# Kernel tuning notes

Hardware: AMD Instinct MI355X
Metric: run time of the kernel (lower is better)

## Reference

```python
import jax, jax.numpy as jnp
import numpy as np

N_NODES = 100000
N_EDGES = 1600000
D_FEAT = 128
N_CLASS = 40
K_HOPS = 2  # nlayers


def setup_inputs() -> dict:
    key = jax.random.key(0)
    k1, k2, k3, k4, k5 = jax.random.split(key, 5)
    src = jax.random.randint(k1, (N_EDGES,), 0, N_NODES)
    dst = jax.random.randint(k2, (N_EDGES,), 0, N_NODES)
    features = jax.random.normal(k3, (N_NODES, D_FEAT), dtype=jnp.float32)
    # positive edge weights (EdgeWeightNorm requires nonnegative)
    edge_weight = jax.random.uniform(k4, (N_EDGES,), dtype=jnp.float32, minval=0.1, maxval=1.0)
    W = jax.random.normal(k5, (D_FEAT, N_CLASS), dtype=jnp.float32) / np.float32(np.sqrt(D_FEAT))
    b = jnp.zeros((N_CLASS,), dtype=jnp.float32)
    return {"features": features, "src": src, "dst": dst,
            "edge_weight": edge_weight, "W": W, "b": b}


def reference(features, src, dst, edge_weight, W, b):
    """SGConv (DGL) with edge_weight: EdgeWeightNorm('both') then k SpMM hops, then fc."""
    n = features.shape[0]
    # EdgeWeightNorm('both'): w_ij / sqrt(out_deg_w(src_i) * in_deg_w(dst_j))
    out_deg = jax.ops.segment_sum(edge_weight, src, num_segments=n)  # weighted out-degree
    in_deg = jax.ops.segment_sum(edge_weight, dst, num_segments=n)   # weighted in-degree
    w = edge_weight * jax.lax.rsqrt(out_deg[src]) * jax.lax.rsqrt(in_deg[dst])  # [E]
    h = features
    for _ in range(K_HOPS):
        # message = h[src] * w ; aggregate = scatter-sum over dst
        h = jax.ops.segment_sum(h[src] * w[:, None], dst, num_segments=n)  # [N, D]
    return h @ W + b  # fc projection [N, C]
```

## Files before the change

### kernel.cpp

```cpp
#include <hip/hip_runtime.h>

#define N_NODES 100000
#define N_EDGES 1600000
#define D_FEAT  128
#define N_CLASS 40
#define ELL_CAP 48

#define QS  10239.6875f
#define DQ  9.765923e-5f
#define FSC  2048.0f
#define FINV (1.0f/2048.0f)
#define CNT_SHIFT 20
#define W_MASK ((1u << CNT_SHIFT) - 1u)

#define RSZ 20000
#define NR 5
#define SLICES 32
#define EPS (N_EDGES/SLICES)
#define HB (NR*SLICES)

#define GEMM2_T ((N_NODES/2)*(N_CLASS/4))
#define GEMM2_B ((GEMM2_T + 1023)/1024)

#define NCH 5

__device__ __forceinline__ float bf_lo(unsigned int u) { return __uint_as_float(u << 16); }
__device__ __forceinline__ float bf_hi(unsigned int u) { return __uint_as_float(u & 0xFFFF0000u); }
__device__ __forceinline__ unsigned int bf_pack2(float a, float b) {
    unsigned int ua = __float_as_uint(a), ub = __float_as_uint(b);
    ua = (ua + 0x7FFFu + ((ua >> 16) & 1u)) >> 16;
    ub = (ub + 0x7FFFu + ((ub >> 16) & 1u)) & 0xFFFF0000u;
    return ua | ub;
}

__global__ __launch_bounds__(1024) void mega1_kernel(
    const int* __restrict__ src, const int* __restrict__ dst, const float* __restrict__ ew,
    const float* __restrict__ f, const float* __restrict__ W,
    unsigned int* __restrict__ dhist, unsigned int* __restrict__ shist,
    unsigned int* __restrict__ g0)
{
    __shared__ unsigned int smem[RSZ];
    const int b = blockIdx.x;
    const int tid = threadIdx.x;

    if (b < 2 * HB) {
        const bool isDst = (b < HB);
        const int b2 = isDst ? b : b - HB;
        const int* idxarr = isDst ? dst : src;
        unsigned int* outh = isDst ? dhist : shist;
        int r = b2 / SLICES, s = b2 - r * SLICES;
        int nb = r * RSZ;
        for (int i = tid; i < RSZ; i += 1024) smem[i] = 0u;
        __syncthreads();
        int e0 = s * EPS;
        const int4*   idx4 = (const int4*)(idxarr + e0);
        const float4* ew4  = (const float4*)(ew + e0);
        const unsigned int cbit = isDst ? (1u << CNT_SHIFT) : 0u;
        for (int i = tid; i < EPS / 8; i += 1024) {
            int4   ia = idx4[2 * i],     ib = idx4[2 * i + 1];
            float4 wa = ew4[2 * i],      wb = ew4[2 * i + 1];
            unsigned int r0 = (unsigned int)(ia.x - nb);
            unsigned int r1 = (unsigned int)(ia.y - nb);
            unsigned int r2 = (unsigned int)(ia.z - nb);
            unsigned int r3 = (unsigned int)(ia.w - nb);
            unsigned int r4 = (unsigned int)(ib.x - nb);
            unsigned int r5 = (unsigned int)(ib.y - nb);
            unsigned int r6 = (unsigned int)(ib.z - nb);
            unsigned int r7 = (unsigned int)(ib.w - nb);
            if (r0 < RSZ) atomicAdd(&smem[r0], cbit | (unsigned int)(wa.x * FSC + 0.5f));
            if (r1 < RSZ) atomicAdd(&smem[r1], cbit | (unsigned int)(wa.y * FSC + 0.5f));
            if (r2 < RSZ) atomicAdd(&smem[r2], cbit | (unsigned int)(wa.z * FSC + 0.5f));
            if (r3 < RSZ) atomicAdd(&smem[r3], cbit | (unsigned int)(wa.w * FSC + 0.5f));
            if (r4 < RSZ) atomicAdd(&smem[r4], cbit | (unsigned int)(wb.x * FSC + 0.5f));
            if (r5 < RSZ) atomicAdd(&smem[r5], cbit | (unsigned int)(wb.y * FSC + 0.5f));
            if (r6 < RSZ) atomicAdd(&smem[r6], cbit | (unsigned int)(wb.z * FSC + 0.5f));
            if (r7 < RSZ) atomicAdd(&smem[r7], cbit | (unsigned int)(wb.w * FSC + 0.5f));
        }
        __syncthreads();
        unsigned int* o = outh + (size_t)b2 * RSZ;
        for (int i = tid; i < RSZ; i += 1024) o[i] = smem[i];
    } else {
        float* Ws = (float*)smem;
        for (int i = tid; i < D_FEAT * N_CLASS; i += 1024) Ws[i] = W[i];
        __syncthreads();
        int idx = (b - 2 * HB) * 1024 + tid;
        if (idx >= GEMM2_T) return;
        int n2 = idx / (N_CLASS / 4);
        int c4i = idx - n2 * (N_CLASS / 4);
        int c4 = c4i * 4;
        int n0 = n2 * 2;
        const float* fr0 = f + (size_t)n0 * D_FEAT;
        const float* fr1 = fr0 + D_FEAT;
        float4 acc0 = {0.f, 0.f, 0.f, 0.f};
        float4 acc1 = {0.f, 0.f, 0.f, 0.f};
#pragma unroll 1
        for (int kq = 0; kq < D_FEAT; kq += 4) {
            float4 fv0 = *(const float4*)(fr0 + kq);
            float4 fv1 = *(const float4*)(fr1 + kq);
#pragma unroll
            for (int j = 0; j < 4; ++j) {
                float fa = (j == 0) ? fv0.x : (j == 1) ? fv0.y : (j == 2) ? fv0.z : fv0.w;
                float fb = (j == 0) ? fv1.x : (j == 1) ? fv1.y : (j == 2) ? fv1.z : fv1.w;
                const float4 wv = *(const float4*)&Ws[(kq + j) * N_CLASS + c4];
                acc0.x = fmaf(fa, wv.x, acc0.x); acc0.y = fmaf(fa, wv.y, acc0.y);
                acc0.z = fmaf(fa, wv.z, acc0.z); acc0.w = fmaf(fa, wv.w, acc0.w);
                acc1.x = fmaf(fb, wv.x, acc1.x); acc1.y = fmaf(fb, wv.y, acc1.y);
                acc1.z = fmaf(fb, wv.z, acc1.z); acc1.w = fmaf(fb, wv.w, acc1.w);
            }
        }
        uint2 p0, p1;
        p0.x = bf_pack2(acc0.x, acc0.y); p0.y = bf_pack2(acc0.z, acc0.w);
        p1.x = bf_pack2(acc1.x, acc1.y); p1.y = bf_pack2(acc1.z, acc1.w);
        *(uint2*)&g0[(size_t)n0 * (N_CLASS / 2) + c4i * 2] = p0;
        *(uint2*)&g0[(size_t)(n0 + 1) * (N_CLASS / 2) + c4i * 2] = p1;
    }
}

__global__ void scan_kernel(const unsigned int* __restrict__ dhist,
                            const unsigned int* __restrict__ shist,
                            unsigned char* __restrict__ base8, int* __restrict__ cnt,
                            float* __restrict__ rs_out, float* __restrict__ rs_in,
                            unsigned int* __restrict__ ell)
{
    int n = blockIdx.x * 256 + threadIdx.x;
    if (n >= N_NODES) return;
    int r = n / RSZ, off = n - r * RSZ;
    const unsigned int* dp = dhist + (size_t)r * SLICES * RSZ + off;
    const unsigned int* sp = shist + (size_t)r * SLICES * RSZ + off;
    unsigned char* b8 = base8 + (size_t)r * SLICES * RSZ + off;
    unsigned int ow = 0, iw = 0, run = 0;
#pragma unroll
    for (int s = 0; s < SLICES; ++s) {
        unsigned int dv = dp[(size_t)s * RSZ];
        ow += sp[(size_t)s * RSZ];
        b8[(size_t)s * RSZ] = (unsigned char)run;
        run += dv >> CNT_SHIFT;
        iw += dv & W_MASK;
    }
    rs_out[n] = ow ? rsqrtf((float)ow * FINV) : 0.f;
    rs_in[n]  = iw ? rsqrtf((float)iw * FINV) : 0.f;
    cnt[n] = (int)run;
    int k  = min((int)run, ELL_CAP);
    int k8 = min((k + 7) & ~7, ELL_CAP);
    unsigned int* row = ell + (size_t)n * ELL_CAP;
    for (int i = k; i < k8; ++i) row[i] = 0u;
}

__global__ __launch_bounds__(1024) void fill_kernel(
    const int* __restrict__ src, const int* __restrict__ dst, const float* __restrict__ ew,
    const unsigned char* __restrict__ base8, const float* __restrict__ rs_out,
    unsigned int* __restrict__ ell)
{
    __shared__ unsigned int lds[RSZ];
    const int r = blockIdx.x & 7;
    const int s = blockIdx.x >> 3;
    if (r >= NR) return;
    const int tid = threadIdx.x;
    const int b2 = r * SLICES + s;
    int nb = r * RSZ;
    const unsigned int* bp = (const unsigned int*)(base8 + (size_t)b2 * RSZ);
    for (int i = tid; i < RSZ / 4; i += 1024) {
        unsigned int v = bp[i];
        lds[4 * i]     = v & 255u;
        lds[4 * i + 1] = (v >> 8) & 255u;
        lds[4 * i + 2] = (v >> 16) & 255u;
        lds[4 * i + 3] = v >> 24;
    }
    __syncthreads();
    int e0 = s * EPS;
    const int4*   d4 = (const int4*)(dst + e0);
    const int4*   s4 = (const int4*)(src + e0);
    const float4* w4 = (const float4*)(ew + e0);
    for (int i = tid; i < EPS / 8; i += 1024) {
        int4   da = d4[2 * i], db = d4[2 * i + 1];
        int4   sa = s4[2 * i], sb = s4[2 * i + 1];
        float4 wa = w4[2 * i], wb = w4[2 * i + 1];
#pragma unroll
        for (int j = 0; j < 8; ++j) {
            int d, sn; float w;
            switch (j) {
                case 0: d = da.x; sn = sa.x; w = wa.x; break;
                case 1: d = da.y; sn = sa.y; w = wa.y; break;
                case 2: d = da.z; sn = sa.z; w = wa.z; break;
                case 3: d = da.w; sn = sa.w; w = wa.w; break;
                case 4: d = db.x; sn = sb.x; w = wb.x; break;
                case 5: d = db.y; sn = sb.y; w = wb.y; break;
                case 6: d = db.z; sn = sb.z; w = wb.z; break;
                default: d = db.w; sn = sb.w; w = wb.w; break;
            }
            unsigned int rr = (unsigned int)(d - nb);
            if (rr < RSZ) {
                unsigned int slot = atomicAdd(&lds[rr], 1u);
                if (slot < ELL_CAP) {
                    int q = (int)(w * rs_out[sn] * QS + 0.5f);
                    q = q > 32767 ? 32767 : q;
                    ell[(size_t)d * ELL_CAP + slot] = ((unsigned int)sn << 15) | (unsigned int)q;
                }
            }
        }
    }
}

__global__ void hop_kernel(const unsigned int* __restrict__ ell, const int* __restrict__ cnt,
                           const float* __restrict__ rs_in, const unsigned int* __restrict__ gin,
                           void* __restrict__ gout, const float* __restrict__ bias)
{
    int t = blockIdx.x * 256 + threadIdx.x;
    if (t >= N_NODES * NCH) return;
    int n = t / NCH;
    int c8 = t - n * NCH;
    int k = min(cnt[n], ELL_CAP);
    k = (k + 7) & ~7;
    const uint4* row4 = (const uint4*)(ell + (size_t)n * ELL_CAP);
    const uint4* gin4 = (const uint4*)gin;
    float a0 = 0.f, a1 = 0.f, a2 = 0.f, a3 = 0.f, a4 = 0.f, a5 = 0.f, a6 = 0.f, a7 = 0.f;
    for (int i = 0; i < k; i += 8) {
        uint4 v0 = row4[i >> 2];
        uint4 v1 = row4[(i >> 2) + 1];
        unsigned int e0 = v0.x, e1 = v0.y, e2 = v0.z, e3 = v0.w;
        unsigned int e4 = v1.x, e5 = v1.y, e6 = v1.z, e7 = v1.w;
        uint4 g0v = gin4[(size_t)(e0 >> 15) * NCH + c8];
        uint4 g1v = gin4[(size_t)(e1 >> 15) * NCH + c8];
        uint4 g2v = gin4[(size_t)(e2 >> 15) * NCH + c8];
        uint4 g3v = gin4[(size_t)(e3 >> 15) * NCH + c8];
        uint4 g4v = gin4[(size_t)(e4 >> 15) * NCH + c8];
        uint4 g5v = gin4[(size_t)(e5 >> 15) * NCH + c8];
        uint4 g6v = gin4[(size_t)(e6 >> 15) * NCH + c8];
        uint4 g7v = gin4[(size_t)(e7 >> 15) * NCH + c8];
        float w0 = (float)(e0 & 32767u) * DQ;
        float w1 = (float)(e1 & 32767u) * DQ;
        float w2 = (float)(e2 & 32767u) * DQ;
        float w3 = (float)(e3 & 32767u) * DQ;
        float w4 = (float)(e4 & 32767u) * DQ;
        float w5 = (float)(e5 & 32767u) * DQ;
        float w6 = (float)(e6 & 32767u) * DQ;
        float w7 = (float)(e7 & 32767u) * DQ;
        a0 = fmaf(w0, bf_lo(g0v.x), a0); a1 = fmaf(w0, bf_hi(g0v.x), a1);
        a2 = fmaf(w0, bf_lo(g0v.y), a2); a3 = fmaf(w0, bf_hi(g0v.y), a3);
        a4 = fmaf(w0, bf_lo(g0v.z), a4); a5 = fmaf(w0, bf_hi(g0v.z), a5);
        a6 = fmaf(w0, bf_lo(g0v.w), a6); a7 = fmaf(w0, bf_hi(g0v.w), a7);
        a0 = fmaf(w1, bf_lo(g1v.x), a0); a1 = fmaf(w1, bf_hi(g1v.x), a1);
        a2 = fmaf(w1, bf_lo(g1v.y), a2); a3 = fmaf(w1, bf_hi(g1v.y), a3);
        a4 = fmaf(w1, bf_lo(g1v.z), a4); a5 = fmaf(w1, bf_hi(g1v.z), a5);
        a6 = fmaf(w1, bf_lo(g1v.w), a6); a7 = fmaf(w1, bf_hi(g1v.w), a7);
        a0 = fmaf(w2, bf_lo(g2v.x), a0); a1 = fmaf(w2, bf_hi(g2v.x), a1);
        a2 = fmaf(w2, bf_lo(g2v.y), a2); a3 = fmaf(w2, bf_hi(g2v.y), a3);
        a4 = fmaf(w2, bf_lo(g2v.z), a4); a5 = fmaf(w2, bf_hi(g2v.z), a5);
        a6 = fmaf(w2, bf_lo(g2v.w), a6); a7 = fmaf(w2, bf_hi(g2v.w), a7);
        a0 = fmaf(w3, bf_lo(g3v.x), a0); a1 = fmaf(w3, bf_hi(g3v.x), a1);
        a2 = fmaf(w3, bf_lo(g3v.y), a2); a3 = fmaf(w3, bf_hi(g3v.y), a3);
        a4 = fmaf(w3, bf_lo(g3v.z), a4); a5 = fmaf(w3, bf_hi(g3v.z), a5);
        a6 = fmaf(w3, bf_lo(g3v.w), a6); a7 = fmaf(w3, bf_hi(g3v.w), a7);
        a0 = fmaf(w4, bf_lo(g4v.x), a0); a1 = fmaf(w4, bf_hi(g4v.x), a1);
        a2 = fmaf(w4, bf_lo(g4v.y), a2); a3 = fmaf(w4, bf_hi(g4v.y), a3);
        a4 = fmaf(w4, bf_lo(g4v.z), a4); a5 = fmaf(w4, bf_hi(g4v.z), a5);
        a6 = fmaf(w4, bf_lo(g4v.w), a6); a7 = fmaf(w4, bf_hi(g4v.w), a7);
        a0 = fmaf(w5, bf_lo(g5v.x), a0); a1 = fmaf(w5, bf_hi(g5v.x), a1);
        a2 = fmaf(w5, bf_lo(g5v.y), a2); a3 = fmaf(w5, bf_hi(g5v.y), a3);
        a4 = fmaf(w5, bf_lo(g5v.z), a4); a5 = fmaf(w5, bf_hi(g5v.z), a5);
        a6 = fmaf(w5, bf_lo(g5v.w), a6); a7 = fmaf(w5, bf_hi(g5v.w), a7);
        a0 = fmaf(w6, bf_lo(g6v.x), a0); a1 = fmaf(w6, bf_hi(g6v.x), a1);
        a2 = fmaf(w6, bf_lo(g6v.y), a2); a3 = fmaf(w6, bf_hi(g6v.y), a3);
        a4 = fmaf(w6, bf_lo(g6v.z), a4); a5 = fmaf(w6, bf_hi(g6v.z), a5);
        a6 = fmaf(w6, bf_lo(g6v.w), a6); a7 = fmaf(w6, bf_hi(g6v.w), a7);
        a0 = fmaf(w7, bf_lo(g7v.x), a0); a1 = fmaf(w7, bf_hi(g7v.x), a1);
        a2 = fmaf(w7, bf_lo(g7v.y), a2); a3 = fmaf(w7, bf_hi(g7v.y), a3);
        a4 = fmaf(w7, bf_lo(g7v.z), a4); a5 = fmaf(w7, bf_hi(g7v.z), a5);
        a6 = fmaf(w7, bf_lo(g7v.w), a6); a7 = fmaf(w7, bf_hi(g7v.w), a7);
    }
    float sc = rs_in[n];
    a0 *= sc; a1 *= sc; a2 *= sc; a3 *= sc; a4 *= sc; a5 *= sc; a6 *= sc; a7 *= sc;
    if (bias) {
        const float4 b0 = *(const float4*)&bias[c8 * 8];
        const float4 b1 = *(const float4*)&bias[c8 * 8 + 4];
        float4 o0 = {a0 + b0.x, a1 + b0.y, a2 + b0.z, a3 + b0.w};
        float4 o1 = {a4 + b1.x, a5 + b1.y, a6 + b1.z, a7 + b1.w};
        float* op = (float*)gout + (size_t)n * N_CLASS + c8 * 8;
        *(float4*)op = o0;
        *(float4*)(op + 4) = o1;
    } else {
        uint4 p;
        p.x = bf_pack2(a0, a1);
        p.y = bf_pack2(a2, a3);
        p.z = bf_pack2(a4, a5);
        p.w = bf_pack2(a6, a7);
        ((uint4*)gout)[(size_t)n * NCH + c8] = p;
    }
}

extern "C" void kernel_launch(void* const* d_in, const int* in_sizes, int n_in,
                              void* d_out, int out_size, void* d_ws, size_t ws_size,
                              hipStream_t stream) {
    const float* features = (const float*)d_in[0];
    const int*   src      = (const int*)d_in[1];
    const int*   dst      = (const int*)d_in[2];
    const float* ew       = (const float*)d_in[3];
    const float* W        = (const float*)d_in[4];
    const float* b        = (const float*)d_in[5];
    float*       out      = (float*)d_out;

    char* ws = (char*)d_ws;
    unsigned int* dhist = (unsigned int*)ws;  ws += (size_t)HB * RSZ * 4;
    unsigned int* shist = (unsigned int*)ws;  ws += (size_t)HB * RSZ * 4;
    unsigned char* base8 = (unsigned char*)ws; ws += (size_t)HB * RSZ;
    int*   cnt    = (int*)ws;    ws += (size_t)N_NODES * 4;
    float* rs_out = (float*)ws;  ws += (size_t)N_NODES * 4;
    float* rs_in  = (float*)ws;  ws += (size_t)N_NODES * 4;
    unsigned int* ell = (unsigned int*)ws; ws += (size_t)N_NODES * ELL_CAP * 4;
    unsigned int* g0  = (unsigned int*)ws;
    unsigned int* g1  = dhist;

    const int B = 256;

    mega1_kernel<<<2 * HB + GEMM2_B, 1024, 0, stream>>>(
        src, dst, ew, features, W, dhist, shist, g0);
    scan_kernel<<<(N_NODES + B - 1) / B, B, 0, stream>>>(
        dhist, shist, base8, cnt, rs_out, rs_in, ell);
    fill_kernel<<<8 * SLICES, 1024, 0, stream>>>(src, dst, ew, base8, rs_out, ell);

    const int HOP_BLOCKS = (N_NODES * NCH + B - 1) / B;
    hop_kernel<<<HOP_BLOCKS, B, 0, stream>>>(ell, cnt, rs_in, g0, (void*)g1, nullptr);
    hop_kernel<<<HOP_BLOCKS, B, 0, stream>>>(ell, cnt, rs_in, g1, (void*)out, b);
}
```

Measured before the change: 252.3 us.

## Split scan across four threads per node and widen GEMM register tile

The per-node scan over 32 histogram slices is split across four threads, each handling 8 slices. Partial sums and counts are combined through shared memory to form the exclusive prefix and the degree normalisers, which adds parallelism and memory-level parallelism to a latency-bound serial loop. The fused GEMM branch now computes four rows per thread instead of two, reusing each W load from LDS across more FMAs. mega1 also gains a launch_bounds occupancy hint of (1024, 8), which can squeeze the register budget.

```diff
diff --git a/kernel.cpp b/kernel.cpp
--- a/kernel.cpp
+++ b/kernel.cpp
@@ -19,8 +19,8 @@
 #define EPS (N_EDGES/SLICES)
 #define HB (NR*SLICES)
 
-#define GEMM2_T ((N_NODES/2)*(N_CLASS/4))
-#define GEMM2_B ((GEMM2_T + 1023)/1024)
+#define GEMM4_T ((N_NODES/4)*(N_CLASS/4))
+#define GEMM4_B ((GEMM4_T + 1023)/1024)
 
 #define NCH 5
 
@@ -33,7 +33,7 @@
     return ua | ub;
 }
 
-__global__ __launch_bounds__(1024) void mega1_kernel(
+__global__ __launch_bounds__(1024, 8) void mega1_kernel(
     const int* __restrict__ src, const int* __restrict__ dst, const float* __restrict__ ew,
     const float* __restrict__ f, const float* __restrict__ W,
     unsigned int* __restrict__ dhist, unsigned int* __restrict__ shist,
@@ -84,66 +84,110 @@
         for (int i = tid; i < D_FEAT * N_CLASS; i += 1024) Ws[i] = W[i];
         __syncthreads();
         int idx = (b - 2 * HB) * 1024 + tid;
-        if (idx >= GEMM2_T) return;
-        int n2 = idx / (N_CLASS / 4);
-        int c4i = idx - n2 * (N_CLASS / 4);
+        if (idx >= GEMM4_T) return;
+        int n4 = idx / (N_CLASS / 4);
+        int c4i = idx - n4 * (N_CLASS / 4);
         int c4 = c4i * 4;
-        int n0 = n2 * 2;
+        int n0 = n4 * 4;
         const float* fr0 = f + (size_t)n0 * D_FEAT;
-        const float* fr1 = fr0 + D_FEAT;
         float4 acc0 = {0.f, 0.f, 0.f, 0.f};
         float4 acc1 = {0.f, 0.f, 0.f, 0.f};
+        float4 acc2 = {0.f, 0.f, 0.f, 0.f};
+        float4 acc3 = {0.f, 0.f, 0.f, 0.f};
 #pragma unroll 1
         for (int kq = 0; kq < D_FEAT; kq += 4) {
             float4 fv0 = *(const float4*)(fr0 + kq);
-            float4 fv1 = *(const float4*)(fr1 + kq);
+            float4 fv1 = *(const float4*)(fr0 + D_FEAT + kq);
+            float4 fv2 = *(const float4*)(fr0 + 2 * D_FEAT + kq);
+            float4 fv3 = *(const float4*)(fr0 + 3 * D_FEAT + kq);
 #pragma unroll
             for (int j = 0; j < 4; ++j) {
                 float fa = (j == 0) ? fv0.x : (j == 1) ? fv0.y : (j == 2) ? fv0.z : fv0.w;
                 float fb = (j == 0) ? fv1.x : (j == 1) ? fv1.y : (j == 2) ? fv1.z : fv1.w;
+                float fc = (j == 0) ? fv2.x : (j == 1) ? fv2.y : (j == 2) ? fv2.z : fv2.w;
+                float fd = (j == 0) ? fv3.x : (j == 1) ? fv3.y : (j == 2) ? fv3.z : fv3.w;
                 const float4 wv = *(const float4*)&Ws[(kq + j) * N_CLASS + c4];
                 acc0.x = fmaf(fa, wv.x, acc0.x); acc0.y = fmaf(fa, wv.y, acc0.y);
                 acc0.z = fmaf(fa, wv.z, acc0.z); acc0.w = fmaf(fa, wv.w, acc0.w);
                 acc1.x = fmaf(fb, wv.x, acc1.x); acc1.y = fmaf(fb, wv.y, acc1.y);
                 acc1.z = fmaf(fb, wv.z, acc1.z); acc1.w = fmaf(fb, wv.w, acc1.w);
+                acc2.x = fmaf(fc, wv.x, acc2.x); acc2.y = fmaf(fc, wv.y, acc2.y);
+                acc2.z = fmaf(fc, wv.z, acc2.z); acc2.w = fmaf(fc, wv.w, acc2.w);
+                acc3.x = fmaf(fd, wv.x, acc3.x); acc3.y = fmaf(fd, wv.y, acc3.y);
+                acc3.z = fmaf(fd, wv.z, acc3.z); acc3.w = fmaf(fd, wv.w, acc3.w);
             }
         }
-        uint2 p0, p1;
+        uint2 p0, p1, p2, p3;
         p0.x = bf_pack2(acc0.x, acc0.y); p0.y = bf_pack2(acc0.z, acc0.w);
         p1.x = bf_pack2(acc1.x, acc1.y); p1.y = bf_pack2(acc1.z, acc1.w);
+        p2.x = bf_pack2(acc2.x, acc2.y); p2.y = bf_pack2(acc2.z, acc2.w);
+        p3.x = bf_pack2(acc3.x, acc3.y); p3.y = bf_pack2(acc3.z, acc3.w);
         *(uint2*)&g0[(size_t)n0 * (N_CLASS / 2) + c4i * 2] = p0;
         *(uint2*)&g0[(size_t)(n0 + 1) * (N_CLASS / 2) + c4i * 2] = p1;
-    }
-}
-
-__global__ void scan_kernel(const unsigned int* __restrict__ dhist,
-                            const unsigned int* __restrict__ shist,
-                            unsigned char* __restrict__ base8, int* __restrict__ cnt,
-                            float* __restrict__ rs_out, float* __restrict__ rs_in,
-                            unsigned int* __restrict__ ell)
+        *(uint2*)&g0[(size_t)(n0 + 2) * (N_CLASS / 2) + c4i * 2] = p2;
+        *(uint2*)&g0[(size_t)(n0 + 3) * (N_CLASS / 2) + c4i * 2] = p3;
+    }
+}
+
+__global__ __launch_bounds__(256) void scan_kernel(
+    const unsigned int* __restrict__ dhist, const unsigned int* __restrict__ shist,
+    unsigned char* __restrict__ base8, int* __restrict__ cnt,
+    float* __restrict__ rs_out, float* __restrict__ rs_in,
+    unsigned int* __restrict__ ell)
 {
-    int n = blockIdx.x * 256 + threadIdx.x;
-    if (n >= N_NODES) return;
-    int r = n / RSZ, off = n - r * RSZ;
-    const unsigned int* dp = dhist + (size_t)r * SLICES * RSZ + off;
-    const unsigned int* sp = shist + (size_t)r * SLICES * RSZ + off;
-    unsigned char* b8 = base8 + (size_t)r * SLICES * RSZ + off;
-    unsigned int ow = 0, iw = 0, run = 0;
-#pragma unroll
-    for (int s = 0; s < SLICES; ++s) {
-        unsigned int dv = dp[(size_t)s * RSZ];
-        ow += sp[(size_t)s * RSZ];
-        b8[(size_t)s * RSZ] = (unsigned char)run;
-        run += dv >> CNT_SHIFT;
-        iw += dv & W_MASK;
-    }
-    rs_out[n] = ow ? rsqrtf((float)ow * FINV) : 0.f;
-    rs_in[n]  = iw ? rsqrtf((float)iw * FINV) : 0.f;
-    cnt[n] = (int)run;
-    int k  = min((int)run, ELL_CAP);
-    int k8 = min((k + 7) & ~7, ELL_CAP);
-    unsigned int* row = ell + (size_t)n * ELL_CAP;
-    for (int i = k; i < k8; ++i) row[i] = 0u;
+    __shared__ unsigned int owp[256], iwp[256], cntp[256];
+    int t = blockIdx.x * 256 + threadIdx.x;
+    int n = t >> 2, q = t & 3;
+    bool valid = n < N_NODES;
+    unsigned int ow = 0, iw = 0, tot = 0;
+    unsigned int c0=0,c1=0,c2=0,c3=0,c4=0,c5=0,c6=0,c7=0;
+    const unsigned int* dp = nullptr;
+    unsigned char* b8 = nullptr;
+    if (valid) {
+        int r = n / RSZ, off = n - r * RSZ;
+        dp = dhist + (size_t)r * SLICES * RSZ + off + (size_t)(q * 8) * RSZ;
+        const unsigned int* sp = shist + (size_t)r * SLICES * RSZ + off + (size_t)(q * 8) * RSZ;
+        b8 = base8 + (size_t)r * SLICES * RSZ + off + (size_t)(q * 8) * RSZ;
+        unsigned int d0 = dp[0],        d1 = dp[(size_t)RSZ],     d2 = dp[(size_t)2*RSZ], d3 = dp[(size_t)3*RSZ];
+        unsigned int d4 = dp[(size_t)4*RSZ], d5 = dp[(size_t)5*RSZ], d6 = dp[(size_t)6*RSZ], d7 = dp[(size_t)7*RSZ];
+        unsigned int s0 = sp[0],        s1 = sp[(size_t)RSZ],     s2 = sp[(size_t)2*RSZ], s3 = sp[(size_t)3*RSZ];
+        unsigned int s4 = sp[(size_t)4*RSZ], s5 = sp[(size_t)5*RSZ], s6 = sp[(size_t)6*RSZ], s7 = sp[(size_t)7*RSZ];
+        ow = s0+s1+s2+s3+s4+s5+s6+s7;
+        iw = (d0&W_MASK)+(d1&W_MASK)+(d2&W_MASK)+(d3&W_MASK)
+           + (d4&W_MASK)+(d5&W_MASK)+(d6&W_MASK)+(d7&W_MASK);
+        c0 = d0>>CNT_SHIFT; c1 = d1>>CNT_SHIFT; c2 = d2>>CNT_SHIFT; c3 = d3>>CNT_SHIFT;
+        c4 = d4>>CNT_SHIFT; c5 = d5>>CNT_SHIFT; c6 = d6>>CNT_SHIFT; c7 = d7>>CNT_SHIFT;
+        tot = c0+c1+c2+c3+c4+c5+c6+c7;
+    }
+    owp[threadIdx.x] = ow; iwp[threadIdx.x] = iw; cntp[threadIdx.x] = tot;
+    __syncthreads();
+    if (!valid) return;
+    int b0 = threadIdx.x & ~3;
+    unsigned int base = 0;
+    if (q > 0) base += cntp[b0];
+    if (q > 1) base += cntp[b0 + 1];
+    if (q > 2) base += cntp[b0 + 2];
+    unsigned int p = base;
+    b8[0] = (unsigned char)p; p += c0;
+    b8[(size_t)RSZ]   = (unsigned char)p; p += c1;
+    b8[(size_t)2*RSZ] = (unsigned char)p; p += c2;
+    b8[(size_t)3*RSZ] = (unsigned char)p; p += c3;
+    b8[(size_t)4*RSZ] = (unsigned char)p; p += c4;
+    b8[(size_t)5*RSZ] = (unsigned char)p; p += c5;
+    b8[(size_t)6*RSZ] = (unsigned char)p; p += c6;
+    b8[(size_t)7*RSZ] = (unsigned char)p;
+    if (q == 0) {
+        unsigned int owt = owp[b0] + owp[b0+1] + owp[b0+2] + owp[b0+3];
+        unsigned int iwt = iwp[b0] + iwp[b0+1] + iwp[b0+2] + iwp[b0+3];
+        unsigned int run = cntp[b0] + cntp[b0+1] + cntp[b0+2] + cntp[b0+3];
+        rs_out[n] = owt ? rsqrtf((float)owt * FINV) : 0.f;
+        rs_in[n]  = iwt ? rsqrtf((float)iwt * FINV) : 0.f;
+        cnt[n] = (int)run;
+        int k  = min((int)run, ELL_CAP);
+        int k8 = min((k + 7) & ~7, ELL_CAP);
+        unsigned int* row = ell + (size_t)n * ELL_CAP;
+        for (int i = k; i < k8; ++i) row[i] = 0u;
+    }
 }
 
 __global__ __launch_bounds__(1024) void fill_kernel(
@@ -312,9 +356,9 @@
 
     const int B = 256;
 
-    mega1_kernel<<<2 * HB + GEMM2_B, 1024, 0, stream>>>(
+    mega1_kernel<<<2 * HB + GEMM4_B, 1024, 0, stream>>>(
         src, dst, ew, features, W, dhist, shist, g0);
-    scan_kernel<<<(N_NODES + B - 1) / B, B, 0, stream>>>(
+    scan_kernel<<<(N_NODES * 4 + B - 1) / B, B, 0, stream>>>(
         dhist, shist, base8, cnt, rs_out, rs_in, ell);
     fill_kernel<<<8 * SLICES, 1024, 0, stream>>>(src, dst, ew, base8, rs_out, ell);
 
```

Result: slower. 271.9 us (+7.8%).
